# Performance work log

Hardware: AMD Instinct MI355X
Metric: run time of the kernel (lower is better)

## Reference

```python
import jax, jax.numpy as jnp
import numpy as np

B, C, N, H = 16, 512, 4096, 512  # batch, visual_channels, visual_flat, hidden_size


def setup_inputs() -> dict:
    key = jax.random.key(0)
    kx, k1, k2, k3, k4 = jax.random.split(key, 5)
    stdv = 1.0 / np.sqrt(H)  # reset_parameters: uniform(-1/sqrt(size(0)), ...), size(0)=H for all weights
    u = lambda k, shape: jax.random.uniform(k, shape, jnp.float32, -stdv, stdv)
    return {
        "visual_inputs": jax.random.normal(kx, (B, C, N), jnp.float32),
        "w_cf": u(k1, (H, N)),  # channel_f: Linear(visual_flat -> hidden)
        "w_cg": u(k2, (H, N)),  # channel_g
        "w_sf": u(k3, (H, C)),  # spatial_f: Conv1d(C -> H, k=1), squeezed
        "w_sg": u(k4, (H, C)),  # spatial_g
    }


def reference(visual_inputs, w_cf, w_cg, w_sf, w_sg):
    x = visual_inputs  # [B, C, N]
    # ---- channel branch: sim[b,c,c'] = <cf[b,c,:], cg[b,c',:]>; summed over dim c then softmax over c'
    cf = jnp.einsum('bcn,hn->bch', x, w_cf)          # [B, C, H]
    cg = jnp.einsum('bcn,hn->bch', x, w_cg)          # [B, C, H]
    # sum_c sim[b,c,c'] = (sum_c cf[b,c,:]) . cg[b,c',:]  -- avoids [B,C,C]
    ch_comp = jnp.einsum('bh,bch->bc', cf.sum(axis=1), cg)        # [B, C]
    channel_mask = jax.nn.softmax(ch_comp, axis=1)[:, :, None]     # [B, C, 1]
    # ---- spatial branch: sim[b,i,j] = <sf[b,:,i], sg[b,:,j]>; summed over dim i then softmax over j
    sf = jnp.einsum('bcn,hc->bhn', x, w_sf)          # [B, H, N]
    sg = jnp.einsum('bcn,hc->bhn', x, w_sg)          # [B, H, N]
    sp_comp = jnp.einsum('bh,bhn->bn', sf.sum(axis=2), sg)         # [B, N]
    spatial_mask = jax.nn.softmax(sp_comp, axis=1)[:, None, :]     # [B, 1, N]
    outputs = x * channel_mask * spatial_mask        # [B, C, N]
    return outputs, channel_mask, spatial_mask
```

## Files before the change

### kernel.cpp

```cpp
#include <hip/hip_runtime.h>

#define Bq 16
#define Cq 512
#define Nq 4096
#define Hq 512

typedef float f32x4 __attribute__((ext_vector_type(4)));

__global__ __launch_bounds__(256) void k1_stats(const float* __restrict__ x,
                                                float* __restrict__ part_xs_n,
                                                float* __restrict__ part_xs_c){
  __shared__ float colred[4][256];
  __shared__ float rowp[4][32][64];
  int blk  = blockIdx.x;
  int b    = blk >> 6;
  int nc   = (blk >> 2) & 15;
  int cq   = blk & 3;
  int wave = threadIdx.x >> 6;
  int lane = threadIdx.x & 63;
  int c0   = cq*128 + wave;
  const float* p = x + ((size_t)b*Cq + c0)*Nq + (nc << 8) + (lane << 2);
  float4 acc = {0.f,0.f,0.f,0.f};
  #pragma unroll 8
  for (int k = 0; k < 32; ++k){
    float4 v = *(const float4*)(p + (size_t)(k*4)*Nq);
    acc.x += v.x; acc.y += v.y; acc.z += v.z; acc.w += v.w;
    rowp[wave][k][lane] = (v.x + v.y) + (v.z + v.w);
  }
  *(float4*)&colred[wave][lane << 2] = acc;
  __syncthreads();
  int t = threadIdx.x;
  part_xs_n[((size_t)(cq*Bq) + b)*Nq + (nc << 8) + t] =
      (colred[0][t] + colred[1][t]) + (colred[2][t] + colred[3][t]);
  if (t < 128){
    const float4* rp4 = (const float4*)&rowp[t & 3][t >> 2][0];
    float4 sv = {0.f,0.f,0.f,0.f};
    #pragma unroll
    for (int j4 = 0; j4 < 16; ++j4){
      float4 vv = rp4[(j4 + t) & 15];
      sv.x += vv.x; sv.y += vv.y; sv.z += vv.z; sv.w += vv.w;
    }
    part_xs_c[((size_t)(b*16 + nc) << 9) + cq*128 + t] =
        (sv.x + sv.y) + (sv.z + sv.w);
  }
}

__global__ __launch_bounds__(256) void k1b_red(const float* __restrict__ part_xs_n,
                                               const float* __restrict__ part_xs_c,
                                               float* __restrict__ xs_n,
                                               float* __restrict__ xs_c){
  int blk = blockIdx.x;
  if (blk < 256){
    int i = (blk << 8) + (int)threadIdx.x;
    float acc = 0.f;
    #pragma unroll
    for (int cq=0; cq<4; ++cq) acc += part_xs_n[(size_t)cq*(Bq*Nq) + i];
    xs_n[i] = acc;
  } else {
    int j = ((blk-256) << 8) + (int)threadIdx.x;
    int b = j >> 9, c = j & 511;
    float acc = 0.f;
    #pragma unroll
    for (int nc=0; nc<16; ++nc) acc += part_xs_c[((size_t)(b*16+nc) << 9) + c];
    xs_c[j] = acc;
  }
}

__global__ __launch_bounds__(256) void k2_s(const float* __restrict__ w_cf,
                                            const float* __restrict__ w_sf,
                                            const float* __restrict__ xs_n,
                                            const float* __restrict__ xs_c,
                                            float* __restrict__ s_cf,
                                            float* __restrict__ s_sf){
  __shared__ float red[4][Bq];
  int blk = blockIdx.x;
  const float* w; const float* src; float* dst; int L;
  if (blk < Hq) { w = w_cf + (size_t)blk*Nq; src = xs_n; dst = s_cf; L = Nq; }
  else          { w = w_sf + (size_t)(blk-Hq)*Cq; src = xs_c; dst = s_sf; L = Cq; }
  int h = blk & (Hq-1);
  int t = threadIdx.x;
  int wave = t >> 6, lane = t & 63;
  float acc[Bq];
  #pragma unroll
  for (int b=0;b<Bq;b++) acc[b]=0.f;
  for (int i0 = t*4; i0 < L; i0 += 1024){
    float4 wv = *(const float4*)(w + i0);
    #pragma unroll
    for (int b=0;b<Bq;b++){
      float4 sv = *(const float4*)(src + (size_t)b*L + i0);
      acc[b] += wv.x*sv.x + wv.y*sv.y + wv.z*sv.z + wv.w*sv.w;
    }
  }
  #pragma unroll
  for (int b=0;b<Bq;b++){
    float v = acc[b];
    #pragma unroll
    for (int off=32; off; off>>=1) v += __shfl_down(v, off, 64);
    if (lane == 0) red[wave][b] = v;
  }
  __syncthreads();
  if (t < Bq)
    dst[(size_t)t*Hq + h] = (red[0][t]+red[1][t])+(red[2][t]+red[3][t]);
}

__global__ __launch_bounds__(256) void k3_v(const float* __restrict__ w_cg,
                                            const float* __restrict__ w_sg,
                                            const float* __restrict__ s_cf,
                                            const float* __restrict__ s_sf,
                                            float* __restrict__ part_cg,
                                            float* __restrict__ part_sg){
  __shared__ float sl[8*64];
  int blk = blockIdx.x;
  const float* w; const float* s; float* dst; int L, jc, hc, bh;
  if (blk < 256){ w=w_cg; s=s_cf; dst=part_cg; L=Nq;
    jc = blk >> 4; hc = (blk >> 1) & 7; bh = blk & 1; }
  else { int k = blk - 256; w=w_sg; s=s_sf; dst=part_sg; L=Cq;
    jc = k >> 4; hc = (k >> 1) & 7; bh = k & 1; }
  int h0 = hc*64, b0 = bh*8;
  for (int i = threadIdx.x; i < 8*64; i += 256){
    int bb = i >> 6, hh = i & 63;
    sl[i] = s[(b0+bb)*Hq + h0 + hh];
  }
  __syncthreads();
  int j = (jc<<8) + (int)threadIdx.x;
  float acc[8];
  #pragma unroll
  for (int bb=0;bb<8;bb++) acc[bb]=0.f;
  #pragma unroll 8
  for (int hh=0; hh<64; ++hh){
    float wv = w[(size_t)(h0+hh)*L + j];
    #pragma unroll
    for (int bb=0;bb<8;bb++) acc[bb] += sl[bb*64+hh]*wv;
  }
  #pragma unroll
  for (int bb=0;bb<8;bb++)
    dst[((size_t)hc*Bq + (b0+bb))*L + j] = acc[bb];
}

__global__ __launch_bounds__(256) void k4_comp(const float* __restrict__ x,
                                               const float* __restrict__ part_cg,
                                               const float* __restrict__ part_sg,
                                               float* __restrict__ part_sp,
                                               float* __restrict__ part_ch){
  __shared__ float colred[4][256];
  __shared__ float rowp[4][32][64];
  __shared__ float vs[128];
  int blk  = blockIdx.x;
  int b    = blk >> 6;
  int nc   = (blk >> 2) & 15;
  int cq   = blk & 3;
  int wave = threadIdx.x >> 6;
  int lane = threadIdx.x & 63;
  int t    = threadIdx.x;
  if (t < 128){
    int c = cq*128 + t;
    float a = 0.f;
    #pragma unroll
    for (int hc=0; hc<8; ++hc) a += part_sg[((size_t)hc*Bq + b)*Cq + c];
    vs[t] = a;
  }
  float4 g = {0.f,0.f,0.f,0.f};
  {
    size_t off = (size_t)b*Nq + (nc << 8) + (lane << 2);
    #pragma unroll
    for (int hc=0; hc<8; ++hc){
      float4 pgv = *(const float4*)(part_cg + (size_t)hc*(Bq*Nq) + off);
      g.x += pgv.x; g.y += pgv.y; g.z += pgv.z; g.w += pgv.w;
    }
  }
  __syncthreads();
  int c0 = cq*128 + wave;
  const float* p = x + ((size_t)b*Cq + c0)*Nq + (nc << 8) + (lane << 2);
  float4 acc = {0.f,0.f,0.f,0.f};
  #pragma unroll 8
  for (int k = 0; k < 32; ++k){
    float4 v = *(const float4*)(p + (size_t)(k*4)*Nq);
    float s = vs[wave + k*4];
    acc.x += v.x*s; acc.y += v.y*s; acc.z += v.z*s; acc.w += v.w*s;
    rowp[wave][k][lane] = v.x*g.x + v.y*g.y + v.z*g.z + v.w*g.w;
  }
  *(float4*)&colred[wave][lane << 2] = acc;
  __syncthreads();
  part_sp[((size_t)(cq*Bq) + b)*Nq + (nc << 8) + t] =
      (colred[0][t] + colred[1][t]) + (colred[2][t] + colred[3][t]);
  if (t < 128){
    const float4* rp4 = (const float4*)&rowp[t & 3][t >> 2][0];
    float4 sv = {0.f,0.f,0.f,0.f};
    #pragma unroll
    for (int j4 = 0; j4 < 16; ++j4){
      float4 vv = rp4[(j4 + t) & 15];
      sv.x += vv.x; sv.y += vv.y; sv.z += vv.z; sv.w += vv.w;
    }
    part_ch[((size_t)(b*16 + nc) << 9) + cq*128 + t] =
        (sv.x + sv.y) + (sv.z + sv.w);
  }
}

__global__ __launch_bounds__(256) void k5_softmax(const float* __restrict__ part_ch,
                                                  const float* __restrict__ part_sp,
                                                  float* __restrict__ out){
  __shared__ float buf[Nq];
  __shared__ float lds[4];
  __shared__ float bcast;
  int blk = blockIdx.x;
  int t = threadIdx.x;
  float* dst; int L;
  const size_t OUT0 = (size_t)Bq*Cq*Nq;
  if (blk < Bq){
    int b = blk; L = Cq;
    for (int c = t; c < Cq; c += 256){
      float s = 0.f;
      #pragma unroll
      for (int nc=0; nc<16; ++nc) s += part_ch[((size_t)(b*16+nc) << 9) + c];
      buf[c] = s;
    }
    dst = out + OUT0 + (size_t)b*Cq;
  } else {
    int b = blk - Bq; L = Nq;
    for (int n = t; n < Nq; n += 256){
      float s = 0.f;
      #pragma unroll
      for (int cq=0; cq<4; ++cq) s += part_sp[((size_t)(cq*Bq)+b)*Nq + n];
      buf[n] = s;
    }
    dst = out + OUT0 + (size_t)Bq*Cq + (size_t)b*Nq;
  }
  __syncthreads();
  float m = -3.4e38f;
  for (int i=t;i<L;i+=256) m = fmaxf(m, buf[i]);
  #pragma unroll
  for (int off=32; off; off>>=1) m = fmaxf(m, __shfl_down(m, off, 64));
  if ((t&63)==0) lds[t>>6]=m;
  __syncthreads();
  if (t==0) bcast = fmaxf(fmaxf(lds[0],lds[1]),fmaxf(lds[2],lds[3]));
  __syncthreads();
  m = bcast;
  float ssum=0.f;
  for (int i=t;i<L;i+=256) ssum += __expf(buf[i]-m);
  #pragma unroll
  for (int off=32; off; off>>=1) ssum += __shfl_down(ssum, off, 64);
  __syncthreads();
  if ((t&63)==0) lds[t>>6]=ssum;
  __syncthreads();
  if (t==0) bcast = 1.f/((lds[0]+lds[1])+(lds[2]+lds[3]));
  __syncthreads();
  float inv = bcast;
  for (int i=t;i<L;i+=256) dst[i] = __expf(buf[i]-m)*inv;
}

__global__ __launch_bounds__(256) void k6_out(const float* __restrict__ x,
                                              float* __restrict__ out){
  const size_t OUT0 = (size_t)Bq*Cq*Nq;
  const float* cm = out + OUT0;
  const float* sm = out + OUT0 + (size_t)Bq*Cq;
  int blk = blockIdx.x;
  int b = blk >> 9;
  size_t rowoff = (size_t)blk * Nq;
  float cmv = cm[blk];
  const float* sp = sm + (size_t)b*Nq;
  int t = threadIdx.x;
  #pragma unroll
  for (int q = 0; q < 4; ++q){
    int n0 = q*1024 + t*4;
    float4 xv = *(const float4*)(x + rowoff + n0);
    float4 sv = *(const float4*)(sp + n0);
    f32x4 o;
    o.x = xv.x*cmv*sv.x; o.y = xv.y*cmv*sv.y;
    o.z = xv.z*cmv*sv.z; o.w = xv.w*cmv*sv.w;
    __builtin_nontemporal_store(o, (f32x4*)(out + rowoff + n0));
  }
}

extern "C" void kernel_launch(void* const* d_in, const int* in_sizes, int n_in,
                              void* d_out, int out_size, void* d_ws, size_t ws_size,
                              hipStream_t stream){
  const float* x    = (const float*)d_in[0];
  const float* w_cf = (const float*)d_in[1];
  const float* w_cg = (const float*)d_in[2];
  const float* w_sf = (const float*)d_in[3];
  const float* w_sg = (const float*)d_in[4];
  float* out = (float*)d_out;

  float* ws = (float*)d_ws;
  float* xs_n = ws;
  float* xs_c = xs_n + Bq*Nq;
  float* s_cf = xs_c + Bq*Cq;
  float* s_sf = s_cf + Bq*Hq;
  float* arenaA = s_sf + Bq*Hq;
  float* part_xs_n = arenaA;
  float* part_xs_c = arenaA + 4*Bq*Nq;
  float* part_cg   = arenaA;
  float* part_sg   = arenaA + 8*Bq*Nq;
  float* arenaB = arenaA + 8*Bq*Nq + 8*Bq*Cq;
  float* part_sp   = arenaB;
  float* part_ch   = arenaB + 4*Bq*Nq;

  k1_stats  <<<1024,  256, 0, stream>>>(x, part_xs_n, part_xs_c);
  k1b_red   <<<288,   256, 0, stream>>>(part_xs_n, part_xs_c, xs_n, xs_c);
  k2_s      <<<2*Hq,  256, 0, stream>>>(w_cf, w_sf, xs_n, xs_c, s_cf, s_sf);
  k3_v      <<<288,   256, 0, stream>>>(w_cg, w_sg, s_cf, s_sf, part_cg, part_sg);
  k4_comp   <<<1024,  256, 0, stream>>>(x, part_cg, part_sg, part_sp, part_ch);
  k5_softmax<<<2*Bq,  256, 0, stream>>>(part_ch, part_sp, out);
  k6_out    <<<Bq*Cq, 256, 0, stream>>>(x, out);
}
```

Baseline: 328.3 us.

## Replace partial-sum buffers and reduction kernel with global atomic accumulation

Partial sums written to workspace and reduced in a separate kernel (k1b_red) or at the next consumer are replaced by float atomicAdds into zeroed accumulators, with a memset added up front. Row sums now use wave shuffles instead of an LDS transpose. The grid for the two x-streaming kernels is doubled to 2048 blocks with half the channels per block. This removes one launch and some partial-buffer traffic. In exchange it adds a memset, atomic contention, and nondeterministic summation order.

Measured after the change: 342.6 us. 4.4% more time.

```diff
diff --git a/kernel.cpp b/kernel.cpp
--- a/kernel.cpp
+++ b/kernel.cpp
@@ -8,62 +8,32 @@
 typedef float f32x4 __attribute__((ext_vector_type(4)));
 
 __global__ __launch_bounds__(256) void k1_stats(const float* __restrict__ x,
-                                                float* __restrict__ part_xs_n,
-                                                float* __restrict__ part_xs_c){
+                                                float* __restrict__ xs_n,
+                                                float* __restrict__ xs_c){
   __shared__ float colred[4][256];
-  __shared__ float rowp[4][32][64];
   int blk  = blockIdx.x;
-  int b    = blk >> 6;
-  int nc   = (blk >> 2) & 15;
-  int cq   = blk & 3;
+  int b    = blk >> 7;
+  int nc   = (blk >> 3) & 15;
+  int cq   = blk & 7;
   int wave = threadIdx.x >> 6;
   int lane = threadIdx.x & 63;
-  int c0   = cq*128 + wave;
+  int c0   = cq*64 + wave;
   const float* p = x + ((size_t)b*Cq + c0)*Nq + (nc << 8) + (lane << 2);
   float4 acc = {0.f,0.f,0.f,0.f};
   #pragma unroll 8
-  for (int k = 0; k < 32; ++k){
+  for (int k = 0; k < 16; ++k){
     float4 v = *(const float4*)(p + (size_t)(k*4)*Nq);
     acc.x += v.x; acc.y += v.y; acc.z += v.z; acc.w += v.w;
-    rowp[wave][k][lane] = (v.x + v.y) + (v.z + v.w);
+    float r = (v.x + v.y) + (v.z + v.w);
+    #pragma unroll
+    for (int off=32; off; off>>=1) r += __shfl_down(r, off, 64);
+    if (lane == 0) atomicAdd(&xs_c[b*Cq + c0 + k*4], r);
   }
   *(float4*)&colred[wave][lane << 2] = acc;
   __syncthreads();
   int t = threadIdx.x;
-  part_xs_n[((size_t)(cq*Bq) + b)*Nq + (nc << 8) + t] =
-      (colred[0][t] + colred[1][t]) + (colred[2][t] + colred[3][t]);
-  if (t < 128){
-    const float4* rp4 = (const float4*)&rowp[t & 3][t >> 2][0];
-    float4 sv = {0.f,0.f,0.f,0.f};
-    #pragma unroll
-    for (int j4 = 0; j4 < 16; ++j4){
-      float4 vv = rp4[(j4 + t) & 15];
-      sv.x += vv.x; sv.y += vv.y; sv.z += vv.z; sv.w += vv.w;
-    }
-    part_xs_c[((size_t)(b*16 + nc) << 9) + cq*128 + t] =
-        (sv.x + sv.y) + (sv.z + sv.w);
-  }
-}
-
-__global__ __launch_bounds__(256) void k1b_red(const float* __restrict__ part_xs_n,
-                                               const float* __restrict__ part_xs_c,
-                                               float* __restrict__ xs_n,
-                                               float* __restrict__ xs_c){
-  int blk = blockIdx.x;
-  if (blk < 256){
-    int i = (blk << 8) + (int)threadIdx.x;
-    float acc = 0.f;
-    #pragma unroll
-    for (int cq=0; cq<4; ++cq) acc += part_xs_n[(size_t)cq*(Bq*Nq) + i];
-    xs_n[i] = acc;
-  } else {
-    int j = ((blk-256) << 8) + (int)threadIdx.x;
-    int b = j >> 9, c = j & 511;
-    float acc = 0.f;
-    #pragma unroll
-    for (int nc=0; nc<16; ++nc) acc += part_xs_c[((size_t)(b*16+nc) << 9) + c];
-    xs_c[j] = acc;
-  }
+  atomicAdd(&xs_n[(size_t)b*Nq + (nc << 8) + t],
+            (colred[0][t] + colred[1][t]) + (colred[2][t] + colred[3][t]));
 }
 
 __global__ __launch_bounds__(256) void k2_s(const float* __restrict__ w_cf,
@@ -107,14 +77,14 @@
                                             const float* __restrict__ w_sg,
                                             const float* __restrict__ s_cf,
                                             const float* __restrict__ s_sf,
-                                            float* __restrict__ part_cg,
-                                            float* __restrict__ part_sg){
+                                            float* __restrict__ v_cg,
+                                            float* __restrict__ v_sg){
   __shared__ float sl[8*64];
   int blk = blockIdx.x;
   const float* w; const float* s; float* dst; int L, jc, hc, bh;
-  if (blk < 256){ w=w_cg; s=s_cf; dst=part_cg; L=Nq;
+  if (blk < 256){ w=w_cg; s=s_cf; dst=v_cg; L=Nq;
     jc = blk >> 4; hc = (blk >> 1) & 7; bh = blk & 1; }
-  else { int k = blk - 256; w=w_sg; s=s_sf; dst=part_sg; L=Cq;
+  else { int k = blk - 256; w=w_sg; s=s_sf; dst=v_sg; L=Cq;
     jc = k >> 4; hc = (k >> 1) & 7; bh = k & 1; }
   int h0 = hc*64, b0 = bh*8;
   for (int i = threadIdx.x; i < 8*64; i += 256){
@@ -134,70 +104,47 @@
   }
   #pragma unroll
   for (int bb=0;bb<8;bb++)
-    dst[((size_t)hc*Bq + (b0+bb))*L + j] = acc[bb];
+    atomicAdd(&dst[(size_t)(b0+bb)*L + j], acc[bb]);
 }
 
 __global__ __launch_bounds__(256) void k4_comp(const float* __restrict__ x,
-                                               const float* __restrict__ part_cg,
-                                               const float* __restrict__ part_sg,
-                                               float* __restrict__ part_sp,
-                                               float* __restrict__ part_ch){
+                                               const float* __restrict__ v_cg,
+                                               const float* __restrict__ v_sg,
+                                               float* __restrict__ sp_comp,
+                                               float* __restrict__ ch_comp){
   __shared__ float colred[4][256];
-  __shared__ float rowp[4][32][64];
-  __shared__ float vs[128];
+  __shared__ float vs[64];
   int blk  = blockIdx.x;
-  int b    = blk >> 6;
-  int nc   = (blk >> 2) & 15;
-  int cq   = blk & 3;
+  int b    = blk >> 7;
+  int nc   = (blk >> 3) & 15;
+  int cq   = blk & 7;
   int wave = threadIdx.x >> 6;
   int lane = threadIdx.x & 63;
   int t    = threadIdx.x;
-  if (t < 128){
-    int c = cq*128 + t;
-    float a = 0.f;
-    #pragma unroll
-    for (int hc=0; hc<8; ++hc) a += part_sg[((size_t)hc*Bq + b)*Cq + c];
-    vs[t] = a;
-  }
-  float4 g = {0.f,0.f,0.f,0.f};
-  {
-    size_t off = (size_t)b*Nq + (nc << 8) + (lane << 2);
-    #pragma unroll
-    for (int hc=0; hc<8; ++hc){
-      float4 pgv = *(const float4*)(part_cg + (size_t)hc*(Bq*Nq) + off);
-      g.x += pgv.x; g.y += pgv.y; g.z += pgv.z; g.w += pgv.w;
-    }
-  }
-  __syncthreads();
-  int c0 = cq*128 + wave;
+  if (t < 64) vs[t] = v_sg[b*Cq + cq*64 + t];
+  float4 g = *(const float4*)(v_cg + (size_t)b*Nq + (nc << 8) + (lane << 2));
+  __syncthreads();
+  int c0 = cq*64 + wave;
   const float* p = x + ((size_t)b*Cq + c0)*Nq + (nc << 8) + (lane << 2);
   float4 acc = {0.f,0.f,0.f,0.f};
   #pragma unroll 8
-  for (int k = 0; k < 32; ++k){
+  for (int k = 0; k < 16; ++k){
     float4 v = *(const float4*)(p + (size_t)(k*4)*Nq);
     float s = vs[wave + k*4];
     acc.x += v.x*s; acc.y += v.y*s; acc.z += v.z*s; acc.w += v.w*s;
-    rowp[wave][k][lane] = v.x*g.x + v.y*g.y + v.z*g.z + v.w*g.w;
+    float r = v.x*g.x + v.y*g.y + v.z*g.z + v.w*g.w;
+    #pragma unroll
+    for (int off=32; off; off>>=1) r += __shfl_down(r, off, 64);
+    if (lane == 0) atomicAdd(&ch_comp[b*Cq + c0 + k*4], r);
   }
   *(float4*)&colred[wave][lane << 2] = acc;
   __syncthreads();
-  part_sp[((size_t)(cq*Bq) + b)*Nq + (nc << 8) + t] =
-      (colred[0][t] + colred[1][t]) + (colred[2][t] + colred[3][t]);
-  if (t < 128){
-    const float4* rp4 = (const float4*)&rowp[t & 3][t >> 2][0];
-    float4 sv = {0.f,0.f,0.f,0.f};
-    #pragma unroll
-    for (int j4 = 0; j4 < 16; ++j4){
-      float4 vv = rp4[(j4 + t) & 15];
-      sv.x += vv.x; sv.y += vv.y; sv.z += vv.z; sv.w += vv.w;
-    }
-    part_ch[((size_t)(b*16 + nc) << 9) + cq*128 + t] =
-        (sv.x + sv.y) + (sv.z + sv.w);
-  }
-}
-
-__global__ __launch_bounds__(256) void k5_softmax(const float* __restrict__ part_ch,
-                                                  const float* __restrict__ part_sp,
+  atomicAdd(&sp_comp[(size_t)b*Nq + (nc << 8) + t],
+            (colred[0][t] + colred[1][t]) + (colred[2][t] + colred[3][t]));
+}
+
+__global__ __launch_bounds__(256) void k5_softmax(const float* __restrict__ ch_comp,
+                                                  const float* __restrict__ sp_comp,
                                                   float* __restrict__ out){
   __shared__ float buf[Nq];
   __shared__ float lds[4];
@@ -208,21 +155,11 @@
   const size_t OUT0 = (size_t)Bq*Cq*Nq;
   if (blk < Bq){
     int b = blk; L = Cq;
-    for (int c = t; c < Cq; c += 256){
-      float s = 0.f;
-      #pragma unroll
-      for (int nc=0; nc<16; ++nc) s += part_ch[((size_t)(b*16+nc) << 9) + c];
-      buf[c] = s;
-    }
+    for (int c = t; c < Cq; c += 256) buf[c] = ch_comp[b*Cq + c];
     dst = out + OUT0 + (size_t)b*Cq;
   } else {
     int b = blk - Bq; L = Nq;
-    for (int n = t; n < Nq; n += 256){
-      float s = 0.f;
-      #pragma unroll
-      for (int cq=0; cq<4; ++cq) s += part_sp[((size_t)(cq*Bq)+b)*Nq + n];
-      buf[n] = s;
-    }
+    for (int n = t; n < Nq; n += 256) buf[n] = sp_comp[(size_t)b*Nq + n];
     dst = out + OUT0 + (size_t)Bq*Cq + (size_t)b*Nq;
   }
   __syncthreads();
@@ -282,24 +219,21 @@
   float* out = (float*)d_out;
 
   float* ws = (float*)d_ws;
-  float* xs_n = ws;
-  float* xs_c = xs_n + Bq*Nq;
-  float* s_cf = xs_c + Bq*Cq;
-  float* s_sf = s_cf + Bq*Hq;
-  float* arenaA = s_sf + Bq*Hq;
-  float* part_xs_n = arenaA;
-  float* part_xs_c = arenaA + 4*Bq*Nq;
-  float* part_cg   = arenaA;
-  float* part_sg   = arenaA + 8*Bq*Nq;
-  float* arenaB = arenaA + 8*Bq*Nq + 8*Bq*Cq;
-  float* part_sp   = arenaB;
-  float* part_ch   = arenaB + 4*Bq*Nq;
-
-  k1_stats  <<<1024,  256, 0, stream>>>(x, part_xs_n, part_xs_c);
-  k1b_red   <<<288,   256, 0, stream>>>(part_xs_n, part_xs_c, xs_n, xs_c);
+  float* xs_n    = ws;
+  float* xs_c    = xs_n    + Bq*Nq;
+  float* v_cg    = xs_c    + Bq*Cq;
+  float* v_sg    = v_cg    + Bq*Nq;
+  float* ch_comp = v_sg    + Bq*Cq;
+  float* sp_comp = ch_comp + Bq*Cq;
+  float* s_cf    = sp_comp + Bq*Nq;
+  float* s_sf    = s_cf    + Bq*Hq;
+  const size_t ZERO_FLOATS = (size_t)2*Bq*Nq + Bq*Nq + 3*(size_t)Bq*Cq;
+
+  hipMemsetAsync(ws, 0, ZERO_FLOATS*sizeof(float), stream);
+  k1_stats  <<<2048,  256, 0, stream>>>(x, xs_n, xs_c);
   k2_s      <<<2*Hq,  256, 0, stream>>>(w_cf, w_sf, xs_n, xs_c, s_cf, s_sf);
-  k3_v      <<<288,   256, 0, stream>>>(w_cg, w_sg, s_cf, s_sf, part_cg, part_sg);
-  k4_comp   <<<1024,  256, 0, stream>>>(x, part_cg, part_sg, part_sp, part_ch);
-  k5_softmax<<<2*Bq,  256, 0, stream>>>(part_ch, part_sp, out);
+  k3_v      <<<288,   256, 0, stream>>>(w_cg, w_sg, s_cf, s_sf, v_cg, v_sg);
+  k4_comp   <<<2048,  256, 0, stream>>>(x, v_cg, v_sg, sp_comp, ch_comp);
+  k5_softmax<<<2*Bq,  256, 0, stream>>>(ch_comp, sp_comp, out);
   k6_out    <<<Bq*Cq, 256, 0, stream>>>(x, out);
 }
```

## Fuse all stages into one cooperative persistent kernel with grid syncs

Applied to the files above, without the earlier changes.

Merges the seven kernel launches into a single cooperative kernel of 1024 blocks, with grid-wide barriers between stages. This removes the launch gaps and tail drain between stages. It also replaces the LDS row-partial reduction with wave shuffle reductions and makes the final output stage process 8 rows per block, reusing the spatial mask loaded into registers. The cost is seven grid barriers with system-scope fences, plus idle blocks in the small stages. It falls back to the old multi-kernel path if occupancy is below 4 blocks per CU or the cooperative launch fails.

Result: no change. 328.5 us (+0.1%).

```diff
diff --git a/kernel.cpp b/kernel.cpp
--- a/kernel.cpp
+++ b/kernel.cpp
@@ -1,4 +1,7 @@
 #include <hip/hip_runtime.h>
+#include <hip/hip_cooperative_groups.h>
+
+namespace cg = cooperative_groups;
 
 #define Bq 16
 #define Cq 512
@@ -7,9 +10,276 @@
 
 typedef float f32x4 __attribute__((ext_vector_type(4)));
 
-__global__ __launch_bounds__(256) void k1_stats(const float* __restrict__ x,
-                                                float* __restrict__ part_xs_n,
-                                                float* __restrict__ part_xs_c){
+#define O_XSN 0
+#define O_XSC (O_XSN + Bq*Nq)
+#define O_SCF (O_XSC + Bq*Cq)
+#define O_SSF (O_SCF + Bq*Hq)
+#define O_ARA (O_SSF + Bq*Hq)
+#define O_PXN (O_ARA)
+#define O_PXC (O_ARA + 4*Bq*Nq)
+#define O_PCG (O_ARA)
+#define O_PSG (O_ARA + 8*Bq*Nq)
+#define O_ARB (O_ARA + 8*Bq*Nq + 8*Bq*Cq)
+#define O_PSP (O_ARB)
+#define O_PCH (O_ARB + 4*Bq*Nq)
+
+__device__ __forceinline__ void gsync(cg::grid_group& g){
+  __syncthreads();
+  if (threadIdx.x == 0) __threadfence_system();
+  g.sync();
+  if (threadIdx.x == 0) __threadfence_system();
+  __syncthreads();
+}
+
+__global__ __launch_bounds__(256, 4) void fused_all(
+    const float* __restrict__ x,
+    const float* __restrict__ w_cf, const float* __restrict__ w_cg,
+    const float* __restrict__ w_sf, const float* __restrict__ w_sg,
+    float* __restrict__ out, float* __restrict__ ws)
+{
+  cg::grid_group grid = cg::this_grid();
+  __shared__ float smem[4101];
+  const int blk  = blockIdx.x;
+  const int t    = threadIdx.x;
+  const int wave = t >> 6;
+  const int lane = t & 63;
+
+  float* part_xs_n = ws + O_PXN;
+  float* part_xs_c = ws + O_PXC;
+  float* xs_n      = ws + O_XSN;
+  float* xs_c      = ws + O_XSC;
+  float* s_cf      = ws + O_SCF;
+  float* s_sf      = ws + O_SSF;
+  float* part_cg   = ws + O_PCG;
+  float* part_sg   = ws + O_PSG;
+  float* part_sp   = ws + O_PSP;
+  float* part_ch   = ws + O_PCH;
+
+  {
+    int b = blk >> 6, nc = (blk >> 2) & 15, cq = blk & 3;
+    int c0 = cq*128 + wave;
+    const float* p = x + ((size_t)b*Cq + c0)*Nq + (nc << 8) + (lane << 2);
+    float* pc = part_xs_c + ((size_t)(b*16 + nc) << 9) + c0;
+    float4 acc = {0.f,0.f,0.f,0.f};
+    #pragma unroll 8
+    for (int k = 0; k < 32; ++k){
+      float4 v = *(const float4*)(p + (size_t)(k*4)*Nq);
+      acc.x += v.x; acc.y += v.y; acc.z += v.z; acc.w += v.w;
+      float r = (v.x + v.y) + (v.z + v.w);
+      #pragma unroll
+      for (int off=32; off; off>>=1) r += __shfl_down(r, off, 64);
+      if (lane == 0) pc[k*4] = r;
+    }
+    *(float4*)&smem[(wave<<8) + (lane<<2)] = acc;
+    __syncthreads();
+    part_xs_n[((size_t)(cq*Bq) + b)*Nq + (nc << 8) + t] =
+        (smem[t] + smem[256+t]) + (smem[512+t] + smem[768+t]);
+  }
+  gsync(grid);
+
+  if (blk < 256){
+    int i = (blk << 8) + t;
+    float a = 0.f;
+    #pragma unroll
+    for (int cq=0; cq<4; ++cq) a += part_xs_n[(size_t)cq*(Bq*Nq) + i];
+    xs_n[i] = a;
+  } else if (blk < 288){
+    int j = ((blk-256) << 8) + t;
+    int b = j >> 9, c = j & 511;
+    float a = 0.f;
+    #pragma unroll
+    for (int nc=0; nc<16; ++nc) a += part_xs_c[((size_t)(b*16+nc) << 9) + c];
+    xs_c[j] = a;
+  }
+  gsync(grid);
+
+  {
+    const float* w; const float* src; float* dst; int L;
+    if (blk < Hq) { w = w_cf + (size_t)blk*Nq; src = xs_n; dst = s_cf; L = Nq; }
+    else          { w = w_sf + (size_t)(blk-Hq)*Cq; src = xs_c; dst = s_sf; L = Cq; }
+    int h = blk & (Hq-1);
+    float acc[Bq];
+    #pragma unroll
+    for (int b=0;b<Bq;b++) acc[b]=0.f;
+    for (int i0 = t*4; i0 < L; i0 += 1024){
+      float4 wv = *(const float4*)(w + i0);
+      #pragma unroll
+      for (int b=0;b<Bq;b++){
+        float4 sv = *(const float4*)(src + (size_t)b*L + i0);
+        acc[b] += wv.x*sv.x + wv.y*sv.y + wv.z*sv.z + wv.w*sv.w;
+      }
+    }
+    float* red = smem;
+    #pragma unroll
+    for (int b=0;b<Bq;b++){
+      float v = acc[b];
+      #pragma unroll
+      for (int off=32; off; off>>=1) v += __shfl_down(v, off, 64);
+      if (lane == 0) red[wave*Bq + b] = v;
+    }
+    __syncthreads();
+    if (t < Bq)
+      dst[(size_t)t*Hq + h] = (red[t]+red[Bq+t])+(red[2*Bq+t]+red[3*Bq+t]);
+  }
+  gsync(grid);
+
+  if (blk < 288){
+    float* sl = smem;
+    const float* w; const float* s; float* dst; int L, jc, hc, bh;
+    if (blk < 256){ w=w_cg; s=s_cf; dst=part_cg; L=Nq;
+      jc = blk >> 4; hc = (blk >> 1) & 7; bh = blk & 1; }
+    else { int k = blk - 256; w=w_sg; s=s_sf; dst=part_sg; L=Cq;
+      jc = k >> 4; hc = (k >> 1) & 7; bh = k & 1; }
+    int h0 = hc*64, b0 = bh*8;
+    for (int i = t; i < 8*64; i += 256){
+      int bb = i >> 6, hh = i & 63;
+      sl[i] = s[(b0+bb)*Hq + h0 + hh];
+    }
+    __syncthreads();
+    int j = (jc<<8) + t;
+    float acc[8];
+    #pragma unroll
+    for (int bb=0;bb<8;bb++) acc[bb]=0.f;
+    #pragma unroll 8
+    for (int hh=0; hh<64; ++hh){
+      float wv = w[(size_t)(h0+hh)*L + j];
+      #pragma unroll
+      for (int bb=0;bb<8;bb++) acc[bb] += sl[bb*64+hh]*wv;
+    }
+    #pragma unroll
+    for (int bb=0;bb<8;bb++)
+      dst[((size_t)hc*Bq + (b0+bb))*L + j] = acc[bb];
+  }
+  gsync(grid);
+
+  {
+    int b = blk >> 6, nc = (blk >> 2) & 15, cq = blk & 3;
+    float* colred = smem;
+    float* vs     = smem + 1024;
+    if (t < 128){
+      int c = cq*128 + t;
+      float a = 0.f;
+      #pragma unroll
+      for (int hc=0; hc<8; ++hc) a += part_sg[((size_t)hc*Bq + b)*Cq + c];
+      vs[t] = a;
+    }
+    float4 g = {0.f,0.f,0.f,0.f};
+    {
+      size_t off = (size_t)b*Nq + (nc << 8) + (lane << 2);
+      #pragma unroll
+      for (int hc=0; hc<8; ++hc){
+        float4 pgv = *(const float4*)(part_cg + (size_t)hc*(Bq*Nq) + off);
+        g.x += pgv.x; g.y += pgv.y; g.z += pgv.z; g.w += pgv.w;
+      }
+    }
+    __syncthreads();
+    int c0 = cq*128 + wave;
+    const float* p = x + ((size_t)b*Cq + c0)*Nq + (nc << 8) + (lane << 2);
+    float* pc = part_ch + ((size_t)(b*16 + nc) << 9) + c0;
+    float4 acc = {0.f,0.f,0.f,0.f};
+    #pragma unroll 8
+    for (int k = 0; k < 32; ++k){
+      float4 v = *(const float4*)(p + (size_t)(k*4)*Nq);
+      float s = vs[wave + k*4];
+      acc.x += v.x*s; acc.y += v.y*s; acc.z += v.z*s; acc.w += v.w*s;
+      float r = v.x*g.x + v.y*g.y + v.z*g.z + v.w*g.w;
+      #pragma unroll
+      for (int off=32; off; off>>=1) r += __shfl_down(r, off, 64);
+      if (lane == 0) pc[k*4] = r;
+    }
+    *(float4*)&colred[(wave<<8) + (lane<<2)] = acc;
+    __syncthreads();
+    part_sp[((size_t)(cq*Bq) + b)*Nq + (nc << 8) + t] =
+        (colred[t] + colred[256+t]) + (colred[512+t] + colred[768+t]);
+  }
+  gsync(grid);
+
+  if (blk < 2*Bq){
+    float* buf   = smem;
+    float* lds4  = smem + 4096;
+    float* bcast = smem + 4100;
+    float* dst; int L;
+    const size_t OUT0 = (size_t)Bq*Cq*Nq;
+    if (blk < Bq){
+      int b = blk; L = Cq;
+      for (int c = t; c < Cq; c += 256){
+        float s = 0.f;
+        #pragma unroll
+        for (int nc=0; nc<16; ++nc) s += part_ch[((size_t)(b*16+nc) << 9) + c];
+        buf[c] = s;
+      }
+      dst = out + OUT0 + (size_t)b*Cq;
+    } else {
+      int b = blk - Bq; L = Nq;
+      for (int n = t; n < Nq; n += 256){
+        float s = 0.f;
+        #pragma unroll
+        for (int cq=0; cq<4; ++cq) s += part_sp[((size_t)(cq*Bq)+b)*Nq + n];
+        buf[n] = s;
+      }
+      dst = out + OUT0 + (size_t)Bq*Cq + (size_t)b*Nq;
+    }
+    __syncthreads();
+    float m = -3.4e38f;
+    for (int i=t;i<L;i+=256) m = fmaxf(m, buf[i]);
+    #pragma unroll
+    for (int off=32; off; off>>=1) m = fmaxf(m, __shfl_down(m, off, 64));
+    if ((t&63)==0) lds4[t>>6]=m;
+    __syncthreads();
+    if (t==0) bcast[0] = fmaxf(fmaxf(lds4[0],lds4[1]),fmaxf(lds4[2],lds4[3]));
+    __syncthreads();
+    m = bcast[0];
+    float ssum=0.f;
+    for (int i=t;i<L;i+=256) ssum += __expf(buf[i]-m);
+    #pragma unroll
+    for (int off=32; off; off>>=1) ssum += __shfl_down(ssum, off, 64);
+    __syncthreads();
+    if ((t&63)==0) lds4[t>>6]=ssum;
+    __syncthreads();
+    if (t==0) bcast[0] = 1.f/((lds4[0]+lds4[1])+(lds4[2]+lds4[3]));
+    __syncthreads();
+    float inv = bcast[0];
+    for (int i=t;i<L;i+=256) dst[i] = __expf(buf[i]-m)*inv;
+  }
+  gsync(grid);
+
+  {
+    const size_t OUT0 = (size_t)Bq*Cq*Nq;
+    const float* cm = out + OUT0;
+    const float* smk = out + OUT0 + (size_t)Bq*Cq;
+    int b = blk >> 6;
+    int cbase = (blk & 63) * 8;
+    const float* sp = smk + (size_t)b*Nq;
+    int n0 = t*4;
+    float4 sv0 = *(const float4*)(sp + n0);
+    float4 sv1 = *(const float4*)(sp + n0 + 1024);
+    float4 sv2 = *(const float4*)(sp + n0 + 2048);
+    float4 sv3 = *(const float4*)(sp + n0 + 3072);
+    #pragma unroll
+    for (int r = 0; r < 8; ++r){
+      int c = cbase + r;
+      size_t ro = ((size_t)b*Cq + c)*Nq;
+      float cmv = cm[b*Cq + c];
+      float4 xv; f32x4 o;
+      xv = *(const float4*)(x + ro + n0);
+      o.x=xv.x*cmv*sv0.x; o.y=xv.y*cmv*sv0.y; o.z=xv.z*cmv*sv0.z; o.w=xv.w*cmv*sv0.w;
+      __builtin_nontemporal_store(o, (f32x4*)(out + ro + n0));
+      xv = *(const float4*)(x + ro + n0 + 1024);
+      o.x=xv.x*cmv*sv1.x; o.y=xv.y*cmv*sv1.y; o.z=xv.z*cmv*sv1.z; o.w=xv.w*cmv*sv1.w;
+      __builtin_nontemporal_store(o, (f32x4*)(out + ro + n0 + 1024));
+      xv = *(const float4*)(x + ro + n0 + 2048);
+      o.x=xv.x*cmv*sv2.x; o.y=xv.y*cmv*sv2.y; o.z=xv.z*cmv*sv2.z; o.w=xv.w*cmv*sv2.w;
+      __builtin_nontemporal_store(o, (f32x4*)(out + ro + n0 + 2048));
+      xv = *(const float4*)(x + ro + n0 + 3072);
+      o.x=xv.x*cmv*sv3.x; o.y=xv.y*cmv*sv3.y; o.z=xv.z*cmv*sv3.z; o.w=xv.w*cmv*sv3.w;
+      __builtin_nontemporal_store(o, (f32x4*)(out + ro + n0 + 3072));
+    }
+  }
+}
+
+__global__ __launch_bounds__(256) void fb_k1(const float* __restrict__ x,
+                                             float* __restrict__ part_xs_n,
+                                             float* __restrict__ part_xs_c){
   __shared__ float colred[4][256];
   __shared__ float rowp[4][32][64];
   int blk  = blockIdx.x;
@@ -45,10 +315,10 @@
   }
 }
 
-__global__ __launch_bounds__(256) void k1b_red(const float* __restrict__ part_xs_n,
-                                               const float* __restrict__ part_xs_c,
-                                               float* __restrict__ xs_n,
-                                               float* __restrict__ xs_c){
+__global__ __launch_bounds__(256) void fb_k1b(const float* __restrict__ part_xs_n,
+                                              const float* __restrict__ part_xs_c,
+                                              float* __restrict__ xs_n,
+                                              float* __restrict__ xs_c){
   int blk = blockIdx.x;
   if (blk < 256){
     int i = (blk << 8) + (int)threadIdx.x;
@@ -66,12 +336,12 @@
   }
 }
 
-__global__ __launch_bounds__(256) void k2_s(const float* __restrict__ w_cf,
-                                            const float* __restrict__ w_sf,
-                                            const float* __restrict__ xs_n,
-                                            const float* __restrict__ xs_c,
-                                            float* __restrict__ s_cf,
-                                            float* __restrict__ s_sf){
+__global__ __launch_bounds__(256) void fb_k2(const float* __restrict__ w_cf,
+                                             const float* __restrict__ w_sf,
+                                             const float* __restrict__ xs_n,
+                                             const float* __restrict__ xs_c,
+                                             float* __restrict__ s_cf,
+                                             float* __restrict__ s_sf){
   __shared__ float red[4][Bq];
   int blk = blockIdx.x;
   const float* w; const float* src; float* dst; int L;
@@ -103,12 +373,12 @@
     dst[(size_t)t*Hq + h] = (red[0][t]+red[1][t])+(red[2][t]+red[3][t]);
 }
 
-__global__ __launch_bounds__(256) void k3_v(const float* __restrict__ w_cg,
-                                            const float* __restrict__ w_sg,
-                                            const float* __restrict__ s_cf,
-                                            const float* __restrict__ s_sf,
-                                            float* __restrict__ part_cg,
-                                            float* __restrict__ part_sg){
+__global__ __launch_bounds__(256) void fb_k3(const float* __restrict__ w_cg,
+                                             const float* __restrict__ w_sg,
+                                             const float* __restrict__ s_cf,
+                                             const float* __restrict__ s_sf,
+                                             float* __restrict__ part_cg,
+                                             float* __restrict__ part_sg){
   __shared__ float sl[8*64];
   int blk = blockIdx.x;
   const float* w; const float* s; float* dst; int L, jc, hc, bh;
@@ -137,11 +407,11 @@
     dst[((size_t)hc*Bq + (b0+bb))*L + j] = acc[bb];
 }
 
-__global__ __launch_bounds__(256) void k4_comp(const float* __restrict__ x,
-                                               const float* __restrict__ part_cg,
-                                               const float* __restrict__ part_sg,
-                                               float* __restrict__ part_sp,
-                                               float* __restrict__ part_ch){
+__global__ __launch_bounds__(256) void fb_k4(const float* __restrict__ x,
+                                             const float* __restrict__ part_cg,
+                                             const float* __restrict__ part_sg,
+                                             float* __restrict__ part_sp,
+                                             float* __restrict__ part_ch){
   __shared__ float colred[4][256];
   __shared__ float rowp[4][32][64];
   __shared__ float vs[128];
@@ -196,9 +466,9 @@
   }
 }
 
-__global__ __launch_bounds__(256) void k5_softmax(const float* __restrict__ part_ch,
-                                                  const float* __restrict__ part_sp,
-                                                  float* __restrict__ out){
+__global__ __launch_bounds__(256) void fb_k5(const float* __restrict__ part_ch,
+                                             const float* __restrict__ part_sp,
+                                             float* __restrict__ out){
   __shared__ float buf[Nq];
   __shared__ float lds[4];
   __shared__ float bcast;
@@ -248,8 +518,8 @@
   for (int i=t;i<L;i+=256) dst[i] = __expf(buf[i]-m)*inv;
 }
 
-__global__ __launch_bounds__(256) void k6_out(const float* __restrict__ x,
-                                              float* __restrict__ out){
+__global__ __launch_bounds__(256) void fb_k6(const float* __restrict__ x,
+                                             float* __restrict__ out){
   const size_t OUT0 = (size_t)Bq*Cq*Nq;
   const float* cm = out + OUT0;
   const float* sm = out + OUT0 + (size_t)Bq*Cq;
@@ -280,26 +550,35 @@
   const float* w_sf = (const float*)d_in[3];
   const float* w_sg = (const float*)d_in[4];
   float* out = (float*)d_out;
-
-  float* ws = (float*)d_ws;
-  float* xs_n = ws;
-  float* xs_c = xs_n + Bq*Nq;
-  float* s_cf = xs_c + Bq*Cq;
-  float* s_sf = s_cf + Bq*Hq;
-  float* arenaA = s_sf + Bq*Hq;
-  float* part_xs_n = arenaA;
-  float* part_xs_c = arenaA + 4*Bq*Nq;
-  float* part_cg   = arenaA;
-  float* part_sg   = arenaA + 8*Bq*Nq;
-  float* arenaB = arenaA + 8*Bq*Nq + 8*Bq*Cq;
-  float* part_sp   = arenaB;
-  float* part_ch   = arenaB + 4*Bq*Nq;
-
-  k1_stats  <<<1024,  256, 0, stream>>>(x, part_xs_n, part_xs_c);
-  k1b_red   <<<288,   256, 0, stream>>>(part_xs_n, part_xs_c, xs_n, xs_c);
-  k2_s      <<<2*Hq,  256, 0, stream>>>(w_cf, w_sf, xs_n, xs_c, s_cf, s_sf);
-  k3_v      <<<288,   256, 0, stream>>>(w_cg, w_sg, s_cf, s_sf, part_cg, part_sg);
-  k4_comp   <<<1024,  256, 0, stream>>>(x, part_cg, part_sg, part_sp, part_ch);
-  k5_softmax<<<2*Bq,  256, 0, stream>>>(part_ch, part_sp, out);
-  k6_out    <<<Bq*Cq, 256, 0, stream>>>(x, out);
-}
+  float* ws  = (float*)d_ws;
+
+  int maxB = 0;
+  hipError_t qerr = hipOccupancyMaxActiveBlocksPerMultiprocessor(
+      &maxB, fused_all, 256, 0);
+  if (qerr == hipSuccess && maxB >= 4){
+    void* args[] = { (void*)&x, (void*)&w_cf, (void*)&w_cg,
+                     (void*)&w_sf, (void*)&w_sg, (void*)&out, (void*)&ws };
+    hipError_t lerr = hipLaunchCooperativeKernel((void*)fused_all, dim3(1024),
+                                                 dim3(256), args, 0, stream);
+    if (lerr == hipSuccess) return;
+  }
+
+  float* xs_n      = ws + O_XSN;
+  float* xs_c      = ws + O_XSC;
+  float* s_cf      = ws + O_SCF;
+  float* s_sf      = ws + O_SSF;
+  float* part_xs_n = ws + O_PXN;
+  float* part_xs_c = ws + O_PXC;
+  float* part_cg   = ws + O_PCG;
+  float* part_sg   = ws + O_PSG;
+  float* part_sp   = ws + O_PSP;
+  float* part_ch   = ws + O_PCH;
+
+  fb_k1 <<<1024,  256, 0, stream>>>(x, part_xs_n, part_xs_c);
+  fb_k1b<<<288,   256, 0, stream>>>(part_xs_n, part_xs_c, xs_n, xs_c);
+  fb_k2 <<<2*Hq,  256, 0, stream>>>(w_cf, w_sf, xs_n, xs_c, s_cf, s_sf);
+  fb_k3 <<<288,   256, 0, stream>>>(w_cg, w_sg, s_cf, s_sf, part_cg, part_sg);
+  fb_k4 <<<1024,  256, 0, stream>>>(x, part_cg, part_sg, part_sp, part_ch);
+  fb_k5 <<<2*Bq,  256, 0, stream>>>(part_ch, part_sp, out);
+  fb_k6 <<<Bq*Cq, 256, 0, stream>>>(x, out);
+}
```

## Fuse partial reductions and softmax into producers via last-block atomic tickets

Applied to the files above, without the earlier changes.

Removes the separate k1b_red and k5_softmax launches. An atomic counter per group lets the last-arriving block of k1_stats and k4_comp perform the final cross-block reduction, and in k4_comp also both softmaxes. Per-row sums that used LDS transposes are now wave shuffle reductions written directly to global memory. The change adds a memset launch, threadfences and atomics, and leaves the final reduction and softmax serialized on a few tail blocks.

Measured after the change: 586.6 us. 1.79x slower.

```diff
diff --git a/kernel.cpp b/kernel.cpp
--- a/kernel.cpp
+++ b/kernel.cpp
@@ -7,62 +7,74 @@
 
 typedef float f32x4 __attribute__((ext_vector_type(4)));
 
+#define O_XSN 0
+#define O_XSC (O_XSN + Bq*Nq)
+#define O_SCF (O_XSC + Bq*Cq)
+#define O_SSF (O_SCF + Bq*Hq)
+#define O_ARA (O_SSF + Bq*Hq)
+#define O_PXN (O_ARA)
+#define O_PXC (O_ARA + 4*Bq*Nq)
+#define O_PCG (O_ARA)
+#define O_PSG (O_ARA + 8*Bq*Nq)
+#define O_ARB (O_ARA + 8*Bq*Nq + 8*Bq*Cq)
+#define O_PSP (O_ARB)
+#define O_PCH (O_ARB + 4*Bq*Nq)
+#define O_CNT (O_ARB + 4*Bq*Nq + 16*Bq*Cq)
+
 __global__ __launch_bounds__(256) void k1_stats(const float* __restrict__ x,
-                                                float* __restrict__ part_xs_n,
-                                                float* __restrict__ part_xs_c){
-  __shared__ float colred[4][256];
-  __shared__ float rowp[4][32][64];
+                                                float* part_xs_n,
+                                                float* part_xs_c,
+                                                float* __restrict__ xs_n,
+                                                float* __restrict__ xs_c,
+                                                int* cnt){
+  __shared__ float colred[1024];
+  __shared__ int tik_n, tik_c;
   int blk  = blockIdx.x;
   int b    = blk >> 6;
   int nc   = (blk >> 2) & 15;
   int cq   = blk & 3;
-  int wave = threadIdx.x >> 6;
-  int lane = threadIdx.x & 63;
+  int t    = threadIdx.x;
+  int wave = t >> 6;
+  int lane = t & 63;
   int c0   = cq*128 + wave;
   const float* p = x + ((size_t)b*Cq + c0)*Nq + (nc << 8) + (lane << 2);
+  float* pc = part_xs_c + ((size_t)(b*16 + nc) << 9) + c0;
   float4 acc = {0.f,0.f,0.f,0.f};
   #pragma unroll 8
   for (int k = 0; k < 32; ++k){
     float4 v = *(const float4*)(p + (size_t)(k*4)*Nq);
     acc.x += v.x; acc.y += v.y; acc.z += v.z; acc.w += v.w;
-    rowp[wave][k][lane] = (v.x + v.y) + (v.z + v.w);
-  }
-  *(float4*)&colred[wave][lane << 2] = acc;
-  __syncthreads();
-  int t = threadIdx.x;
+    float r = (v.x + v.y) + (v.z + v.w);
+    #pragma unroll
+    for (int off=32; off; off>>=1) r += __shfl_down(r, off, 64);
+    if (lane == 0) pc[k*4] = r;
+  }
+  *(float4*)&colred[(wave<<8) + (lane<<2)] = acc;
+  __syncthreads();
   part_xs_n[((size_t)(cq*Bq) + b)*Nq + (nc << 8) + t] =
-      (colred[0][t] + colred[1][t]) + (colred[2][t] + colred[3][t]);
-  if (t < 128){
-    const float4* rp4 = (const float4*)&rowp[t & 3][t >> 2][0];
-    float4 sv = {0.f,0.f,0.f,0.f};
-    #pragma unroll
-    for (int j4 = 0; j4 < 16; ++j4){
-      float4 vv = rp4[(j4 + t) & 15];
-      sv.x += vv.x; sv.y += vv.y; sv.z += vv.z; sv.w += vv.w;
-    }
-    part_xs_c[((size_t)(b*16 + nc) << 9) + cq*128 + t] =
-        (sv.x + sv.y) + (sv.z + sv.w);
-  }
-}
-
-__global__ __launch_bounds__(256) void k1b_red(const float* __restrict__ part_xs_n,
-                                               const float* __restrict__ part_xs_c,
-                                               float* __restrict__ xs_n,
-                                               float* __restrict__ xs_c){
-  int blk = blockIdx.x;
-  if (blk < 256){
-    int i = (blk << 8) + (int)threadIdx.x;
-    float acc = 0.f;
-    #pragma unroll
-    for (int cq=0; cq<4; ++cq) acc += part_xs_n[(size_t)cq*(Bq*Nq) + i];
-    xs_n[i] = acc;
-  } else {
-    int j = ((blk-256) << 8) + (int)threadIdx.x;
-    int b = j >> 9, c = j & 511;
-    float acc = 0.f;
-    #pragma unroll
-    for (int nc=0; nc<16; ++nc) acc += part_xs_c[((size_t)(b*16+nc) << 9) + c];
-    xs_c[j] = acc;
+      (colred[t] + colred[256+t]) + (colred[512+t] + colred[768+t]);
+
+  __threadfence();
+  if (t == 0){
+    tik_n = atomicAdd(&cnt[b*16 + nc], 1);
+    tik_c = atomicAdd(&cnt[256 + b*4 + cq], 1);
+  }
+  __syncthreads();
+  if (tik_n == 3){
+    __threadfence();
+    int i = b*Nq + (nc << 8) + t;
+    float a = 0.f;
+    #pragma unroll
+    for (int q = 0; q < 4; ++q) a += part_xs_n[(size_t)q*(Bq*Nq) + i];
+    xs_n[i] = a;
+  }
+  if (tik_c == 15 && t < 128){
+    __threadfence();
+    int c = cq*128 + t;
+    float a = 0.f;
+    #pragma unroll
+    for (int q = 0; q < 16; ++q) a += part_xs_c[((size_t)(b*16 + q) << 9) + c];
+    xs_c[b*Cq + c] = a;
   }
 }
 
@@ -140,112 +152,129 @@
 __global__ __launch_bounds__(256) void k4_comp(const float* __restrict__ x,
                                                const float* __restrict__ part_cg,
                                                const float* __restrict__ part_sg,
-                                               float* __restrict__ part_sp,
-                                               float* __restrict__ part_ch){
-  __shared__ float colred[4][256];
-  __shared__ float rowp[4][32][64];
-  __shared__ float vs[128];
+                                               float* part_sp,
+                                               float* part_ch,
+                                               float* __restrict__ out,
+                                               int* cnt){
+  __shared__ float smem[4224];
+  __shared__ int tik;
   int blk  = blockIdx.x;
   int b    = blk >> 6;
   int nc   = (blk >> 2) & 15;
   int cq   = blk & 3;
-  int wave = threadIdx.x >> 6;
-  int lane = threadIdx.x & 63;
   int t    = threadIdx.x;
-  if (t < 128){
-    int c = cq*128 + t;
-    float a = 0.f;
-    #pragma unroll
-    for (int hc=0; hc<8; ++hc) a += part_sg[((size_t)hc*Bq + b)*Cq + c];
-    vs[t] = a;
-  }
-  float4 g = {0.f,0.f,0.f,0.f};
+  int wave = t >> 6;
+  int lane = t & 63;
+  const size_t OUT0 = (size_t)Bq*Cq*Nq;
   {
-    size_t off = (size_t)b*Nq + (nc << 8) + (lane << 2);
-    #pragma unroll
-    for (int hc=0; hc<8; ++hc){
-      float4 pgv = *(const float4*)(part_cg + (size_t)hc*(Bq*Nq) + off);
-      g.x += pgv.x; g.y += pgv.y; g.z += pgv.z; g.w += pgv.w;
-    }
-  }
-  __syncthreads();
-  int c0 = cq*128 + wave;
-  const float* p = x + ((size_t)b*Cq + c0)*Nq + (nc << 8) + (lane << 2);
-  float4 acc = {0.f,0.f,0.f,0.f};
-  #pragma unroll 8
-  for (int k = 0; k < 32; ++k){
-    float4 v = *(const float4*)(p + (size_t)(k*4)*Nq);
-    float s = vs[wave + k*4];
-    acc.x += v.x*s; acc.y += v.y*s; acc.z += v.z*s; acc.w += v.w*s;
-    rowp[wave][k][lane] = v.x*g.x + v.y*g.y + v.z*g.z + v.w*g.w;
-  }
-  *(float4*)&colred[wave][lane << 2] = acc;
-  __syncthreads();
-  part_sp[((size_t)(cq*Bq) + b)*Nq + (nc << 8) + t] =
-      (colred[0][t] + colred[1][t]) + (colred[2][t] + colred[3][t]);
-  if (t < 128){
-    const float4* rp4 = (const float4*)&rowp[t & 3][t >> 2][0];
-    float4 sv = {0.f,0.f,0.f,0.f};
-    #pragma unroll
-    for (int j4 = 0; j4 < 16; ++j4){
-      float4 vv = rp4[(j4 + t) & 15];
-      sv.x += vv.x; sv.y += vv.y; sv.z += vv.z; sv.w += vv.w;
-    }
-    part_ch[((size_t)(b*16 + nc) << 9) + cq*128 + t] =
-        (sv.x + sv.y) + (sv.z + sv.w);
-  }
-}
-
-__global__ __launch_bounds__(256) void k5_softmax(const float* __restrict__ part_ch,
-                                                  const float* __restrict__ part_sp,
-                                                  float* __restrict__ out){
-  __shared__ float buf[Nq];
-  __shared__ float lds[4];
-  __shared__ float bcast;
-  int blk = blockIdx.x;
-  int t = threadIdx.x;
-  float* dst; int L;
-  const size_t OUT0 = (size_t)Bq*Cq*Nq;
-  if (blk < Bq){
-    int b = blk; L = Cq;
+    float* colred = smem;
+    float* vs     = smem + 1024;
+    if (t < 128){
+      int c = cq*128 + t;
+      float a = 0.f;
+      #pragma unroll
+      for (int hc=0; hc<8; ++hc) a += part_sg[((size_t)hc*Bq + b)*Cq + c];
+      vs[t] = a;
+    }
+    float4 g = {0.f,0.f,0.f,0.f};
+    {
+      size_t off = (size_t)b*Nq + (nc << 8) + (lane << 2);
+      #pragma unroll
+      for (int hc=0; hc<8; ++hc){
+        float4 pgv = *(const float4*)(part_cg + (size_t)hc*(Bq*Nq) + off);
+        g.x += pgv.x; g.y += pgv.y; g.z += pgv.z; g.w += pgv.w;
+      }
+    }
+    __syncthreads();
+    int c0 = cq*128 + wave;
+    const float* p = x + ((size_t)b*Cq + c0)*Nq + (nc << 8) + (lane << 2);
+    float* pch = part_ch + ((size_t)(b*16 + nc) << 9) + c0;
+    float4 acc = {0.f,0.f,0.f,0.f};
+    #pragma unroll 8
+    for (int k = 0; k < 32; ++k){
+      float4 v = *(const float4*)(p + (size_t)(k*4)*Nq);
+      float s = vs[wave + k*4];
+      acc.x += v.x*s; acc.y += v.y*s; acc.z += v.z*s; acc.w += v.w*s;
+      float r = v.x*g.x + v.y*g.y + v.z*g.z + v.w*g.w;
+      #pragma unroll
+      for (int off=32; off; off>>=1) r += __shfl_down(r, off, 64);
+      if (lane == 0) pch[k*4] = r;
+    }
+    *(float4*)&colred[(wave<<8) + (lane<<2)] = acc;
+    __syncthreads();
+    part_sp[((size_t)(cq*Bq) + b)*Nq + (nc << 8) + t] =
+        (colred[t] + colred[256+t]) + (colred[512+t] + colred[768+t]);
+  }
+  __threadfence();
+  if (t == 0) tik = atomicAdd(&cnt[320 + b], 1);
+  __syncthreads();
+  if (tik == 63){
+    __threadfence();
+    float* buf   = smem;
+    float* lds4  = smem + 4096;
+    float* bcast = smem + 4100;
+    for (int n = t; n < Nq; n += 256){
+      float s = 0.f;
+      #pragma unroll
+      for (int q=0; q<4; ++q) s += part_sp[((size_t)(q*Bq)+b)*Nq + n];
+      buf[n] = s;
+    }
+    __syncthreads();
+    {
+      float* dst = out + OUT0 + (size_t)Bq*Cq + (size_t)b*Nq;
+      float m = -3.4e38f;
+      for (int i=t;i<Nq;i+=256) m = fmaxf(m, buf[i]);
+      #pragma unroll
+      for (int off=32; off; off>>=1) m = fmaxf(m, __shfl_down(m, off, 64));
+      if ((t&63)==0) lds4[t>>6]=m;
+      __syncthreads();
+      if (t==0) bcast[0] = fmaxf(fmaxf(lds4[0],lds4[1]),fmaxf(lds4[2],lds4[3]));
+      __syncthreads();
+      m = bcast[0];
+      float ssum=0.f;
+      for (int i=t;i<Nq;i+=256) ssum += __expf(buf[i]-m);
+      #pragma unroll
+      for (int off=32; off; off>>=1) ssum += __shfl_down(ssum, off, 64);
+      __syncthreads();
+      if ((t&63)==0) lds4[t>>6]=ssum;
+      __syncthreads();
+      if (t==0) bcast[0] = 1.f/((lds4[0]+lds4[1])+(lds4[2]+lds4[3]));
+      __syncthreads();
+      float inv = bcast[0];
+      for (int i=t;i<Nq;i+=256) dst[i] = __expf(buf[i]-m)*inv;
+    }
+    __syncthreads();
     for (int c = t; c < Cq; c += 256){
       float s = 0.f;
       #pragma unroll
-      for (int nc=0; nc<16; ++nc) s += part_ch[((size_t)(b*16+nc) << 9) + c];
+      for (int q=0; q<16; ++q) s += part_ch[((size_t)(b*16+q) << 9) + c];
       buf[c] = s;
     }
-    dst = out + OUT0 + (size_t)b*Cq;
-  } else {
-    int b = blk - Bq; L = Nq;
-    for (int n = t; n < Nq; n += 256){
-      float s = 0.f;
-      #pragma unroll
-      for (int cq=0; cq<4; ++cq) s += part_sp[((size_t)(cq*Bq)+b)*Nq + n];
-      buf[n] = s;
-    }
-    dst = out + OUT0 + (size_t)Bq*Cq + (size_t)b*Nq;
-  }
-  __syncthreads();
-  float m = -3.4e38f;
-  for (int i=t;i<L;i+=256) m = fmaxf(m, buf[i]);
-  #pragma unroll
-  for (int off=32; off; off>>=1) m = fmaxf(m, __shfl_down(m, off, 64));
-  if ((t&63)==0) lds[t>>6]=m;
-  __syncthreads();
-  if (t==0) bcast = fmaxf(fmaxf(lds[0],lds[1]),fmaxf(lds[2],lds[3]));
-  __syncthreads();
-  m = bcast;
-  float ssum=0.f;
-  for (int i=t;i<L;i+=256) ssum += __expf(buf[i]-m);
-  #pragma unroll
-  for (int off=32; off; off>>=1) ssum += __shfl_down(ssum, off, 64);
-  __syncthreads();
-  if ((t&63)==0) lds[t>>6]=ssum;
-  __syncthreads();
-  if (t==0) bcast = 1.f/((lds[0]+lds[1])+(lds[2]+lds[3]));
-  __syncthreads();
-  float inv = bcast;
-  for (int i=t;i<L;i+=256) dst[i] = __expf(buf[i]-m)*inv;
+    __syncthreads();
+    {
+      float* dst = out + OUT0 + (size_t)b*Cq;
+      float m = -3.4e38f;
+      for (int i=t;i<Cq;i+=256) m = fmaxf(m, buf[i]);
+      #pragma unroll
+      for (int off=32; off; off>>=1) m = fmaxf(m, __shfl_down(m, off, 64));
+      if ((t&63)==0) lds4[t>>6]=m;
+      __syncthreads();
+      if (t==0) bcast[0] = fmaxf(fmaxf(lds4[0],lds4[1]),fmaxf(lds4[2],lds4[3]));
+      __syncthreads();
+      m = bcast[0];
+      float ssum=0.f;
+      for (int i=t;i<Cq;i+=256) ssum += __expf(buf[i]-m);
+      #pragma unroll
+      for (int off=32; off; off>>=1) ssum += __shfl_down(ssum, off, 64);
+      __syncthreads();
+      if ((t&63)==0) lds4[t>>6]=ssum;
+      __syncthreads();
+      if (t==0) bcast[0] = 1.f/((lds4[0]+lds4[1])+(lds4[2]+lds4[3]));
+      __syncthreads();
+      float inv = bcast[0];
+      for (int i=t;i<Cq;i+=256) dst[i] = __expf(buf[i]-m)*inv;
+    }
+  }
 }
 
 __global__ __launch_bounds__(256) void k6_out(const float* __restrict__ x,
@@ -280,26 +309,24 @@
   const float* w_sf = (const float*)d_in[3];
   const float* w_sg = (const float*)d_in[4];
   float* out = (float*)d_out;
-
-  float* ws = (float*)d_ws;
-  float* xs_n = ws;
-  float* xs_c = xs_n + Bq*Nq;
-  float* s_cf = xs_c + Bq*Cq;
-  float* s_sf = s_cf + Bq*Hq;
-  float* arenaA = s_sf + Bq*Hq;
-  float* part_xs_n = arenaA;
-  float* part_xs_c = arenaA + 4*Bq*Nq;
-  float* part_cg   = arenaA;
-  float* part_sg   = arenaA + 8*Bq*Nq;
-  float* arenaB = arenaA + 8*Bq*Nq + 8*Bq*Cq;
-  float* part_sp   = arenaB;
-  float* part_ch   = arenaB + 4*Bq*Nq;
-
-  k1_stats  <<<1024,  256, 0, stream>>>(x, part_xs_n, part_xs_c);
-  k1b_red   <<<288,   256, 0, stream>>>(part_xs_n, part_xs_c, xs_n, xs_c);
-  k2_s      <<<2*Hq,  256, 0, stream>>>(w_cf, w_sf, xs_n, xs_c, s_cf, s_sf);
-  k3_v      <<<288,   256, 0, stream>>>(w_cg, w_sg, s_cf, s_sf, part_cg, part_sg);
-  k4_comp   <<<1024,  256, 0, stream>>>(x, part_cg, part_sg, part_sp, part_ch);
-  k5_softmax<<<2*Bq,  256, 0, stream>>>(part_ch, part_sp, out);
-  k6_out    <<<Bq*Cq, 256, 0, stream>>>(x, out);
-}
+  float* ws  = (float*)d_ws;
+
+  float* xs_n      = ws + O_XSN;
+  float* xs_c      = ws + O_XSC;
+  float* s_cf      = ws + O_SCF;
+  float* s_sf      = ws + O_SSF;
+  float* part_xs_n = ws + O_PXN;
+  float* part_xs_c = ws + O_PXC;
+  float* part_cg   = ws + O_PCG;
+  float* part_sg   = ws + O_PSG;
+  float* part_sp   = ws + O_PSP;
+  float* part_ch   = ws + O_PCH;
+  int*   cnt       = (int*)(ws + O_CNT);
+
+  hipMemsetAsync(cnt, 0, 336*sizeof(int), stream);
+  k1_stats<<<1024,  256, 0, stream>>>(x, part_xs_n, part_xs_c, xs_n, xs_c, cnt);
+  k2_s    <<<2*Hq,  256, 0, stream>>>(w_cf, w_sf, xs_n, xs_c, s_cf, s_sf);
+  k3_v    <<<288,   256, 0, stream>>>(w_cg, w_sg, s_cf, s_sf, part_cg, part_sg);
+  k4_comp <<<1024,  256, 0, stream>>>(x, part_cg, part_sg, part_sp, part_ch, out, cnt);
+  k6_out  <<<Bq*Cq, 256, 0, stream>>>(x, out);
+}
```
